# Kernel optimization log

Hardware: AMD Instinct MI355X
Metric: run time of the kernel (lower is better)

## Reference

```python
import jax, jax.numpy as jnp
import numpy as np
from jax import lax

B, N = 2048, 8192


def setup_inputs() -> dict:
    key = jax.random.key(0)
    k1, k2 = jax.random.split(key)
    # alpha in [0, 0.3) keeps the tridiagonal system diagonally dominant in fp32
    alpha = 0.3 * jax.random.uniform(k1, (B, N), dtype=jnp.float32)
    f = jax.random.normal(k2, (N,), dtype=jnp.float32)
    return {"alpha": alpha, "f": f}


def _thomas(a, b, c, f):
    """Batched Thomas solve. a: (B,N-1) sub, b: (B,N) diag, c: (B,N-1) super, f: (B,N)."""
    Bn = b.shape[0]
    a_p = jnp.pad(a, ((0, 0), (1, 0)))  # a_0 := 0
    c_p = jnp.pad(c, ((0, 0), (0, 1)))  # c_{N-1} := 0

    def fwd(carry, x):
        cp_prev, dp_prev = carry
        ai, bi, ci, fi = x
        denom = bi - ai * cp_prev
        cp = ci / denom
        dp = (fi - ai * dp_prev) / denom
        return (cp, dp), (cp, dp)

    zeros = jnp.zeros((Bn,), dtype=b.dtype)
    _, (cps, dps) = lax.scan(fwd, (zeros, zeros), (a_p.T, b.T, c_p.T, f.T))

    def bwd(u_next, x):
        cp, dp = x
        u = dp - cp * u_next
        return u, u

    _, us = lax.scan(bwd, zeros, (cps, dps), reverse=True)
    return us.T  # (B, N)


def reference(alpha, f):
    # Tridiagonal matrix A(alpha)
    a = alpha[:, :-1] ** 2                      # subdiagonal
    b = 1.0 + alpha ** 3                        # diagonal
    c = alpha[:, 1:] ** 2 + 2.0 * alpha[:, 1:]  # superdiagonal
    f_b = jnp.broadcast_to(f, alpha.shape)      # (B, N)
    return _thomas(a, b, c, f_b)
```

## Files before the change

### kernel.cpp

```cpp
#include <hip/hip_runtime.h>


#define NN 8192
#define TB 256
#define CH 32

__device__ __forceinline__ float frcp(float x) { return __builtin_amdgcn_rcpf(x); }

__global__ __launch_bounds__(TB, 2)
void thomas_scan_kernel(const float* __restrict__ alpha,
                        const float* __restrict__ fvec,
                        float* __restrict__ out)
{
    __shared__ float sm0[TB], sm1[TB], sm2[TB], sm3[TB], sm4[TB], sm5[TB], sm6[TB];
    __shared__ float sA[TB], sB[TB];

    const int t   = threadIdx.x;
    const int row = blockIdx.x;
    const float* __restrict__ arow = alpha + (size_t)row * NN;
    const int base = t * CH;

    float va[CH], vf[CH];
    {
        const float4* a4 = reinterpret_cast<const float4*>(arow + base);
        const float4* f4 = reinterpret_cast<const float4*>(fvec + base);
        #pragma unroll
        for (int k = 0; k < CH / 4; ++k) {
            float4 x = a4[k];
            va[4*k+0] = x.x; va[4*k+1] = x.y; va[4*k+2] = x.z; va[4*k+3] = x.w;
            float4 y = f4[k];
            vf[4*k+0] = y.x; vf[4*k+1] = y.y; vf[4*k+2] = y.z; vf[4*k+3] = y.w;
        }
    }
    const float aL = (t > 0)      ? arow[base - 1]  : 0.0f;
    const float aR = (t < TB - 1) ? arow[base + CH] : 0.0f;

    float p = 1.f, q = 0.f, r = 0.f, s = 1.f, tt = 0.f, u = 0.f, v = 1.f;
    #pragma unroll
    for (int k = 0; k < CH; ++k) {
        const float am1 = (k == 0)      ? aL : va[k-1];
        const float ap1 = (k == CH - 1) ? aR : va[k+1];
        const float ai = am1 * am1;
        const float bi = 1.0f + va[k] * va[k] * va[k];
        const float ci = ap1 * (ap1 + 2.0f);
        const float fi = vf[k];
        const float np = ci * u;
        const float nq = ci * v;
        const float nr = fi * u - ai * r;
        const float ns = -ai * s;
        const float nt = fi * v - ai * tt;
        const float nu = bi * u - ai * p;
        const float nv = bi * v - ai * q;
        p = np; q = nq; r = nr; s = ns; tt = nt; u = nu; v = nv;
    }
    {
        const float inv = frcp(v);
        p *= inv; q *= inv; r *= inv; s *= inv; tt *= inv; u *= inv; v = 1.0f;
    }
    sm0[t] = p; sm1[t] = q; sm2[t] = r; sm3[t] = s; sm4[t] = tt; sm5[t] = u; sm6[t] = v;
    __syncthreads();

    #pragma unroll
    for (int off = 1; off < TB; off <<= 1) {
        float p1=0, q1=0, r1=0, s1=0, t1=0, u1=0, v1=0;
        const bool act = (t >= off);
        if (act) {
            p1 = sm0[t-off]; q1 = sm1[t-off]; r1 = sm2[t-off]; s1 = sm3[t-off];
            t1 = sm4[t-off]; u1 = sm5[t-off]; v1 = sm6[t-off];
        }
        __syncthreads();
        if (act) {
            const float np = p*p1 + q*u1;
            const float nq = p*q1 + q*v1;
            const float nr = r*p1 + s*r1 + tt*u1;
            const float ns = s*s1;
            const float nt = r*q1 + s*t1 + tt*v1;
            const float nu = u*p1 + v*u1;
            const float nv = u*q1 + v*v1;
            const float inv = frcp(nv);
            p = np*inv; q = nq*inv; r = nr*inv; s = ns*inv; tt = nt*inv; u = nu*inv; v = 1.0f;
        }
        sm0[t] = p; sm1[t] = q; sm2[t] = r; sm3[t] = s; sm4[t] = tt; sm5[t] = u; sm6[t] = v;
        __syncthreads();
    }

    float cp, dp;
    if (t == 0) { cp = 0.0f; dp = 0.0f; }
    else {
        const float rz = frcp(sm6[t-1]);
        cp = sm1[t-1] * rz;
        dp = sm4[t-1] * rz;
    }

    float cpv[CH], dpv[CH];
    #pragma unroll
    for (int k = 0; k < CH; ++k) {
        const float am1 = (k == 0)      ? aL : va[k-1];
        const float ap1 = (k == CH - 1) ? aR : va[k+1];
        const float ai = am1 * am1;
        const float bi = 1.0f + va[k] * va[k] * va[k];
        const float ci = ap1 * (ap1 + 2.0f);
        const float fi = vf[k];
        const float rd = frcp(bi - ai * cp);
        cp = ci * rd;
        dp = (fi - ai * dp) * rd;
        cpv[k] = cp;
        dpv[k] = dp;
    }

    float A = 1.0f, Bb = 0.0f;
    #pragma unroll
    for (int k = CH - 1; k >= 0; --k) {
        Bb = dpv[k] - cpv[k] * Bb;
        A  = -cpv[k] * A;
    }
    sA[t] = A; sB[t] = Bb;
    __syncthreads();
    #pragma unroll
    for (int off = 1; off < TB; off <<= 1) {
        float A1 = 0.f, B1 = 0.f;
        const bool act = (t + off < TB);
        if (act) { A1 = sA[t + off]; B1 = sB[t + off]; }
        __syncthreads();
        if (act) { Bb = A * B1 + Bb; A = A * A1; }
        sA[t] = A; sB[t] = Bb;
        __syncthreads();
    }
    const float u_in = (t == TB - 1) ? 0.0f : sB[t + 1];

    float uv[CH];
    float un = u_in;
    #pragma unroll
    for (int k = CH - 1; k >= 0; --k) {
        un = dpv[k] - cpv[k] * un;
        uv[k] = un;
    }
    float4* o4 = reinterpret_cast<float4*>(out + (size_t)row * NN + base);
    #pragma unroll
    for (int k = 0; k < CH / 4; ++k) {
        o4[k] = make_float4(uv[4*k+0], uv[4*k+1], uv[4*k+2], uv[4*k+3]);
    }
}

extern "C" void kernel_launch(void* const* d_in, const int* in_sizes, int n_in,
                              void* d_out, int out_size, void* d_ws, size_t ws_size,
                              hipStream_t stream) {
    const float* alpha = (const float*)d_in[0];
    const float* fvec  = (const float*)d_in[1];
    float* out = (float*)d_out;
    const int nrows = out_size / NN;
    thomas_scan_kernel<<<nrows, TB, 0, stream>>>(alpha, fvec, out);
}
```

Before: 139.5 us.

## Replace shared-memory block scans with wavefront shuffle scans and 512-thread blocks

Swaps both Hillis-Steele scans, which ran through shared memory with many __syncthreads barriers, for intra-wavefront __shfl_up/__shfl_down scans followed by a small serial combine across wave totals. Each scan now needs a single block barrier, and v is normalised to 1 so it no longer has to be carried. Blocks grow to 512 threads with 16 elements per thread, which gives more parallelism per row and fewer registers per thread. The cost is a serial loop over up to 8 wave totals and a shorter sequential chunk per thread.

```diff
diff --git a/kernel.cpp b/kernel.cpp
--- a/kernel.cpp
+++ b/kernel.cpp
@@ -2,21 +2,24 @@
 
 
 #define NN 8192
-#define TB 256
-#define CH 32
+#define TB 512
+#define CH 16
+#define NWAVE (TB/64)
 
 __device__ __forceinline__ float frcp(float x) { return __builtin_amdgcn_rcpf(x); }
 
-__global__ __launch_bounds__(TB, 2)
+__global__ __launch_bounds__(TB, 4)
 void thomas_scan_kernel(const float* __restrict__ alpha,
                         const float* __restrict__ fvec,
                         float* __restrict__ out)
 {
-    __shared__ float sm0[TB], sm1[TB], sm2[TB], sm3[TB], sm4[TB], sm5[TB], sm6[TB];
-    __shared__ float sA[TB], sB[TB];
+    __shared__ float wtot[NWAVE][6];
+    __shared__ float btot[NWAVE][2];
 
-    const int t   = threadIdx.x;
-    const int row = blockIdx.x;
+    const int t    = threadIdx.x;
+    const int lane = t & 63;
+    const int wid  = t >> 6;
+    const int row  = blockIdx.x;
     const float* __restrict__ arow = alpha + (size_t)row * NN;
     const int base = t * CH;
 
@@ -27,112 +30,128 @@
         #pragma unroll
         for (int k = 0; k < CH / 4; ++k) {
             float4 x = a4[k];
-            va[4*k+0] = x.x; va[4*k+1] = x.y; va[4*k+2] = x.z; va[4*k+3] = x.w;
+            va[4*k+0]=x.x; va[4*k+1]=x.y; va[4*k+2]=x.z; va[4*k+3]=x.w;
             float4 y = f4[k];
-            vf[4*k+0] = y.x; vf[4*k+1] = y.y; vf[4*k+2] = y.z; vf[4*k+3] = y.w;
+            vf[4*k+0]=y.x; vf[4*k+1]=y.y; vf[4*k+2]=y.z; vf[4*k+3]=y.w;
         }
     }
     const float aL = (t > 0)      ? arow[base - 1]  : 0.0f;
     const float aR = (t < TB - 1) ? arow[base + CH] : 0.0f;
 
-    float p = 1.f, q = 0.f, r = 0.f, s = 1.f, tt = 0.f, u = 0.f, v = 1.f;
+    float p=1.f, q=0.f, r=0.f, s=1.f, tt=0.f, u=0.f, v=1.f;
     #pragma unroll
     for (int k = 0; k < CH; ++k) {
         const float am1 = (k == 0)      ? aL : va[k-1];
         const float ap1 = (k == CH - 1) ? aR : va[k+1];
         const float ai = am1 * am1;
-        const float bi = 1.0f + va[k] * va[k] * va[k];
+        const float bi = 1.0f + va[k]*va[k]*va[k];
         const float ci = ap1 * (ap1 + 2.0f);
         const float fi = vf[k];
-        const float np = ci * u;
-        const float nq = ci * v;
-        const float nr = fi * u - ai * r;
-        const float ns = -ai * s;
-        const float nt = fi * v - ai * tt;
-        const float nu = bi * u - ai * p;
-        const float nv = bi * v - ai * q;
-        p = np; q = nq; r = nr; s = ns; tt = nt; u = nu; v = nv;
+        const float np = ci*u,        nq = ci*v;
+        const float nr = fi*u - ai*r, ns = -ai*s, nt = fi*v - ai*tt;
+        const float nu = bi*u - ai*p, nv = bi*v - ai*q;
+        p=np; q=nq; r=nr; s=ns; tt=nt; u=nu; v=nv;
     }
-    {
-        const float inv = frcp(v);
-        p *= inv; q *= inv; r *= inv; s *= inv; tt *= inv; u *= inv; v = 1.0f;
+    { const float inv = frcp(v); p*=inv; q*=inv; r*=inv; s*=inv; tt*=inv; u*=inv; }
+
+    #pragma unroll
+    for (int off = 1; off < 64; off <<= 1) {
+        const float p1 = __shfl_up(p, off);
+        const float q1 = __shfl_up(q, off);
+        const float r1 = __shfl_up(r, off);
+        const float s1 = __shfl_up(s, off);
+        const float t1 = __shfl_up(tt, off);
+        const float u1 = __shfl_up(u, off);
+        if (lane >= off) {
+            const float np = p*p1 + q*u1;
+            const float nq = p*q1 + q;
+            const float nr = r*p1 + s*r1 + tt*u1;
+            const float ns = s*s1;
+            const float nt = r*q1 + s*t1 + tt;
+            const float nu = u*p1 + u1;
+            const float nv = u*q1 + 1.0f;
+            const float inv = frcp(nv);
+            p=np*inv; q=nq*inv; r=nr*inv; s=ns*inv; tt=nt*inv; u=nu*inv;
+        }
     }
-    sm0[t] = p; sm1[t] = q; sm2[t] = r; sm3[t] = s; sm4[t] = tt; sm5[t] = u; sm6[t] = v;
+    if (lane == 63) {
+        wtot[wid][0]=p; wtot[wid][1]=q; wtot[wid][2]=r;
+        wtot[wid][3]=s; wtot[wid][4]=tt; wtot[wid][5]=u;
+    }
     __syncthreads();
 
-    #pragma unroll
-    for (int off = 1; off < TB; off <<= 1) {
-        float p1=0, q1=0, r1=0, s1=0, t1=0, u1=0, v1=0;
-        const bool act = (t >= off);
-        if (act) {
-            p1 = sm0[t-off]; q1 = sm1[t-off]; r1 = sm2[t-off]; s1 = sm3[t-off];
-            t1 = sm4[t-off]; u1 = sm5[t-off]; v1 = sm6[t-off];
-        }
-        __syncthreads();
-        if (act) {
-            const float np = p*p1 + q*u1;
-            const float nq = p*q1 + q*v1;
-            const float nr = r*p1 + s*r1 + tt*u1;
-            const float ns = s*s1;
-            const float nt = r*q1 + s*t1 + tt*v1;
-            const float nu = u*p1 + v*u1;
-            const float nv = u*q1 + v*v1;
-            const float inv = frcp(nv);
-            p = np*inv; q = nq*inv; r = nr*inv; s = ns*inv; tt = nt*inv; u = nu*inv; v = 1.0f;
-        }
-        sm0[t] = p; sm1[t] = q; sm2[t] = r; sm3[t] = s; sm4[t] = tt; sm5[t] = u; sm6[t] = v;
-        __syncthreads();
+    float ep=__shfl_up(p,1), eq=__shfl_up(q,1), er=__shfl_up(r,1),
+          es=__shfl_up(s,1), et=__shfl_up(tt,1), eu=__shfl_up(u,1);
+    if (lane == 0) { ep=1.f; eq=0.f; er=0.f; es=1.f; et=0.f; eu=0.f; }
+
+    float Pp=1.f, Pq=0.f, Pr=0.f, Ps=1.f, Pt=0.f, Pu=0.f;
+    for (int w = 0; w < wid; ++w) {
+        const float p1=wtot[w][0], q1=wtot[w][1], r1=wtot[w][2],
+                    s1=wtot[w][3], t1=wtot[w][4], u1=wtot[w][5];
+        const float np = p1*Pp + q1*Pu;
+        const float nq = p1*Pq + q1;
+        const float nr = r1*Pp + s1*Pr + t1*Pu;
+        const float ns = s1*Ps;
+        const float nt = r1*Pq + s1*Pt + t1;
+        const float nu = u1*Pp + Pu;
+        const float nv = u1*Pq + 1.0f;
+        const float inv = frcp(nv);
+        Pp=np*inv; Pq=nq*inv; Pr=nr*inv; Ps=ns*inv; Pt=nt*inv; Pu=nu*inv;
+    }
+    float Eq, Et;
+    {
+        const float nq = ep*Pq + eq;
+        const float nt = er*Pq + es*Pt + et;
+        const float nv = eu*Pq + 1.0f;
+        const float inv = frcp(nv);
+        Eq = nq*inv; Et = nt*inv;
     }
 
-    float cp, dp;
-    if (t == 0) { cp = 0.0f; dp = 0.0f; }
-    else {
-        const float rz = frcp(sm6[t-1]);
-        cp = sm1[t-1] * rz;
-        dp = sm4[t-1] * rz;
-    }
-
+    float cp = Eq, dp = Et;
     float cpv[CH], dpv[CH];
     #pragma unroll
     for (int k = 0; k < CH; ++k) {
         const float am1 = (k == 0)      ? aL : va[k-1];
         const float ap1 = (k == CH - 1) ? aR : va[k+1];
         const float ai = am1 * am1;
-        const float bi = 1.0f + va[k] * va[k] * va[k];
+        const float bi = 1.0f + va[k]*va[k]*va[k];
         const float ci = ap1 * (ap1 + 2.0f);
-        const float fi = vf[k];
-        const float rd = frcp(bi - ai * cp);
+        const float rd = frcp(bi - ai*cp);
         cp = ci * rd;
-        dp = (fi - ai * dp) * rd;
-        cpv[k] = cp;
-        dpv[k] = dp;
+        dp = (vf[k] - ai*dp) * rd;
+        cpv[k] = cp; dpv[k] = dp;
     }
 
     float A = 1.0f, Bb = 0.0f;
     #pragma unroll
     for (int k = CH - 1; k >= 0; --k) {
-        Bb = dpv[k] - cpv[k] * Bb;
-        A  = -cpv[k] * A;
+        Bb = dpv[k] - cpv[k]*Bb;
+        A  = -cpv[k]*A;
     }
-    sA[t] = A; sB[t] = Bb;
+    #pragma unroll
+    for (int off = 1; off < 64; off <<= 1) {
+        const float A1 = __shfl_down(A, off);
+        const float B1 = __shfl_down(Bb, off);
+        if (lane < 64 - off) { Bb = A*B1 + Bb; A = A*A1; }
+    }
+    if (lane == 0) { btot[wid][0] = A; btot[wid][1] = Bb; }
     __syncthreads();
-    #pragma unroll
-    for (int off = 1; off < TB; off <<= 1) {
-        float A1 = 0.f, B1 = 0.f;
-        const bool act = (t + off < TB);
-        if (act) { A1 = sA[t + off]; B1 = sB[t + off]; }
-        __syncthreads();
-        if (act) { Bb = A * B1 + Bb; A = A * A1; }
-        sA[t] = A; sB[t] = Bb;
-        __syncthreads();
+
+    float eA = __shfl_down(A, 1), eB = __shfl_down(Bb, 1);
+    if (lane == 63) { eA = 1.0f; eB = 0.0f; }
+    float SA = 1.0f, SB = 0.0f;
+    for (int w = NWAVE - 1; w > wid; --w) {
+        const float A1 = btot[w][0], B1 = btot[w][1];
+        SB = A1*SB + B1;
+        SA = A1*SA;
     }
-    const float u_in = (t == TB - 1) ? 0.0f : sB[t + 1];
+    const float u_in = eA*SB + eB;
 
     float uv[CH];
     float un = u_in;
     #pragma unroll
     for (int k = CH - 1; k >= 0; --k) {
-        un = dpv[k] - cpv[k] * un;
+        un = dpv[k] - cpv[k]*un;
         uv[k] = un;
     }
     float4* o4 = reinterpret_cast<float4*>(out + (size_t)row * NN + base);
```

Result: faster. 129.7 us (-7.0%).
